# Kernel optimization log

Measured on AMD Instinct MI355X. Metric: run time of the kernel, lower is better.

Reference implementation:

```python
import jax, jax.numpy as jnp
import numpy as np

M = 4096        # reference column size (init kwarg m)
TAU = 1.0       # temperature
SLICE_LEN = 4096


def setup_inputs() -> dict:
    key = jax.random.key(0)
    scores = jax.random.normal(key, (4, 131072), dtype=jnp.float32)
    return {"scores": scores}


def reference(scores):
    B, n = scores.shape
    m = min(M, n)
    # global top-m (sorted descending, matching torch.topk sorted=True)
    ref_val, ref_idx = jax.lax.top_k(scores, m)          # (B, m), (B, m)

    n_chunks = n // SLICE_LEN
    # (n_chunks, B, SLICE_LEN): scan over token chunks so only one
    # (B, SLICE_LEN, m) pairwise block is live at a time, as in the torch loop.
    chunks = jnp.swapaxes(scores.reshape(B, n_chunks, SLICE_LEN), 0, 1)

    def step(_, slice_scores):
        # pairwise = -|s_i - ref_j| / tau  -> softmax over m -> argmax -> gather
        pairwise = -jnp.abs(slice_scores[..., None] - ref_val[:, None, :]) / TAU
        P_hat = jax.nn.softmax(pairwise, axis=-1)        # (B, SLICE_LEN, m)
        col_rank = jnp.argmax(P_hat, axis=-1)            # (B, SLICE_LEN)
        perm_slice = jnp.take_along_axis(ref_idx, col_rank, axis=1)
        return None, perm_slice

    _, perms = jax.lax.scan(step, None, chunks)          # (n_chunks, B, SLICE_LEN)
    perm = jnp.swapaxes(perms, 0, 1).reshape(B, n)       # (B, n) int32 indices
    return perm
```

## Files before the change

### kernel.cpp

```cpp
#include <hip/hip_runtime.h>
#include <stdint.h>

#define BROWS 4
#define NCOLS 131072
#define MREF  4096
#define HIST_BITS 13
#define NBUCK (1 << HIST_BITS)
#define USHIFT (32 - HIST_BITS)
#define CAP 6144
#define HIST_BLK_PER_ROW 8
#define NPART 32
#define PQUOTA 192
#define PARTCAP 1024

__device__ __forceinline__ uint32_t orderable(float f) {
    uint32_t u = __float_as_uint(f);
    return (u & 0x80000000u) ? ~u : (u | 0x80000000u);
}
__device__ __forceinline__ float unorderable(uint32_t u) {
    uint32_t b = (u & 0x80000000u) ? (u & 0x7FFFFFFFu) : ~u;
    return __uint_as_float(b);
}

__global__ void k_zero(uint32_t* hist) {
    int i = blockIdx.x * blockDim.x + threadIdx.x;
    int tot = BROWS * NBUCK;
    for (; i < tot; i += gridDim.x * blockDim.x) hist[i] = 0u;
}

__global__ void k_hist(const float* __restrict__ sc, uint32_t* __restrict__ hist) {
    __shared__ uint32_t h[NBUCK];
    for (int t = threadIdx.x; t < NBUCK; t += blockDim.x) h[t] = 0u;
    __syncthreads();
    int row  = blockIdx.x / HIST_BLK_PER_ROW;
    int part = blockIdx.x % HIST_BLK_PER_ROW;
    const int CHUNK = NCOLS / HIST_BLK_PER_ROW;
    const float* p = sc + row * NCOLS + part * CHUNK;
    for (int c = threadIdx.x; c < CHUNK; c += blockDim.x) {
        uint32_t u = orderable(p[c]);
        atomicAdd(&h[u >> USHIFT], 1u);
    }
    __syncthreads();
    uint32_t* g = hist + (row << HIST_BITS);
    for (int t = threadIdx.x; t < NBUCK; t += blockDim.x) {
        uint32_t v = h[t];
        if (v) atomicAdd(&g[t], v);
    }
}

__global__ void k_thresh(const uint32_t* __restrict__ hist, uint32_t* __restrict__ Hrow,
                         int* __restrict__ Bs, uint32_t* __restrict__ pcur,
                         uint32_t* __restrict__ pse) {
    __shared__ uint32_t inc[256];
    int row = blockIdx.x;
    const uint32_t* h = hist + (row << HIST_BITS);
    int bhi = NBUCK - 1 - (int)threadIdx.x * 32;
    uint32_t run = 0;
    for (int k = 0; k < 32; ++k) run += h[bhi - k];
    inc[threadIdx.x] = run;
    __syncthreads();
    for (int off = 1; off < 256; off <<= 1) {
        uint32_t v = (threadIdx.x >= (uint32_t)off) ? inc[threadIdx.x - off] : 0u;
        __syncthreads();
        inc[threadIdx.x] += v;
        __syncthreads();
    }
    uint32_t excl = inc[threadIdx.x] - run;

    if (threadIdx.x == 0) {
        Bs[row * NPART + 0] = NBUCK;
        pcur[row * NPART + 0] = 0u;
        pse[row * (NPART + 1) + 0] = 0u;
    }

    uint32_t cum = excl;
    for (int k = 0; k < 32; ++k) {
        int b = bhi - k;
        uint32_t prev = cum;
        cum += h[b];
        if (prev < (uint32_t)MREF) {
            uint32_t plo = prev / PQUOTA + 1u;
            uint32_t phi = cum / PQUOTA;
            if (phi > (uint32_t)(NPART - 1)) phi = (uint32_t)(NPART - 1);
            for (uint32_t p = plo; p <= phi; ++p) {
                uint32_t st = prev; if (st > (uint32_t)CAP) st = (uint32_t)CAP;
                Bs[row * NPART + p] = b;
                pcur[row * NPART + p] = st;
                pse[row * (NPART + 1) + p] = st;
            }
            if (cum >= (uint32_t)MREF) {
                uint32_t T = cum; if (T > (uint32_t)CAP) T = (uint32_t)CAP;
                Hrow[row] = (uint32_t)b;
                pse[row * (NPART + 1) + NPART] = T;
                uint32_t pstart = cum / PQUOTA + 1u;
                for (uint32_t p = pstart; p < (uint32_t)NPART; ++p) {
                    Bs[row * NPART + p] = b - 1;
                    pcur[row * NPART + p] = T;
                    pse[row * (NPART + 1) + p] = T;
                }
            }
        }
    }
}

__global__ void k_compact(const float* __restrict__ sc, const uint32_t* __restrict__ Hrow,
                          const int* __restrict__ Bs, uint32_t* __restrict__ pcur,
                          uint64_t* __restrict__ cand) {
    __shared__ int bsL[NPART];
    __shared__ uint32_t cntP[NPART];
    __shared__ uint32_t baseP[NPART];
    int row = blockIdx.x >> 7;
    int base = (blockIdx.x & 127) << 10;
    uint32_t H = Hrow[row];
    if (threadIdx.x < NPART) {
        bsL[threadIdx.x] = Bs[row * NPART + threadIdx.x];
        cntP[threadIdx.x] = 0u;
    }
    __syncthreads();
    const float* p = sc + row * NCOLS + base;

    uint32_t myu[4], mycol[4], myr[4];
    int myp[4];
    uint32_t n = 0;
    for (int k = 0; k < 4; ++k) {
        int c = (int)threadIdx.x + (k << 8);
        uint32_t u = orderable(p[c]);
        uint32_t b = u >> USHIFT;
        if (b >= H) {
            int pp = 0;
            for (int q = 1; q < NPART; ++q) pp += ((int)b <= bsL[q]) ? 1 : 0;
            myu[n] = u; mycol[n] = (uint32_t)(base + c); myp[n] = pp;
            myr[n] = atomicAdd(&cntP[pp], 1u);
            ++n;
        }
    }
    __syncthreads();
    if (threadIdx.x < NPART)
        baseP[threadIdx.x] = atomicAdd(&pcur[row * NPART + threadIdx.x], cntP[threadIdx.x]);
    __syncthreads();
    uint64_t* cr = cand + (size_t)row * CAP;
    for (uint32_t k = 0; k < n; ++k) {
        uint32_t idx = baseP[myp[k]] + myr[k];
        if (idx < (uint32_t)CAP)
            cr[idx] = ((uint64_t)(~myu[k]) << 32) | mycol[k];
    }
}

#define BITONIC_SORT(PP)                                                        \
    for (uint32_t i = threadIdx.x; i < (uint32_t)(PP); i += blockDim.x)         \
        lds[i] = (i < n) ? seg[i] : ~0ULL;                                      \
    __syncthreads();                                                            \
    for (uint32_t k = 2; k <= (uint32_t)(PP); k <<= 1) {                        \
        for (uint32_t j = k >> 1; j > 0; j >>= 1) {                             \
            for (uint32_t i = threadIdx.x; i < (uint32_t)(PP); i += blockDim.x) { \
                uint32_t ixj = i ^ j;                                           \
                if (ixj > i) {                                                  \
                    uint64_t a = lds[i], bb = lds[ixj];                         \
                    bool up = ((i & k) == 0);                                   \
                    if ((a > bb) == up) { lds[i] = bb; lds[ixj] = a; }          \
                }                                                               \
            }                                                                   \
            __syncthreads();                                                    \
        }                                                                       \
    }

__global__ void k_psort(const uint32_t* __restrict__ pse, uint64_t* __restrict__ cand,
                        float* __restrict__ rv, uint32_t* __restrict__ ri) {
    __shared__ uint64_t lds[PARTCAP];
    int row = blockIdx.x >> 5;
    int pp  = blockIdx.x & 31;
    uint32_t start = pse[row * (NPART + 1) + pp];
    uint32_t end   = pse[row * (NPART + 1) + pp + 1];
    if (end > (uint32_t)CAP) end = (uint32_t)CAP;
    uint32_t n = (end > start) ? (end - start) : 0u;
    if (n > (uint32_t)PARTCAP) n = (uint32_t)PARTCAP;
    uint64_t* seg = cand + (size_t)row * CAP + start;
    if (n <= 256u) {
        BITONIC_SORT(256)
    } else if (n <= 512u) {
        BITONIC_SORT(512)
    } else {
        BITONIC_SORT(1024)
    }
    for (uint32_t i = threadIdx.x; i < n; i += blockDim.x) {
        uint32_t gpos = start + i;
        if (gpos < (uint32_t)MREF) {
            uint64_t key = lds[i];
            uint32_t u = ~(uint32_t)(key >> 32);
            rv[row * MREF + gpos] = unorderable(u);
            ri[row * MREF + gpos] = (uint32_t)(key & 0xFFFFFFFFu);
        }
    }
}

__global__ void k_map(const float* __restrict__ sc, const float* __restrict__ rv,
                      const uint32_t* __restrict__ ri, int* __restrict__ out) {
    __shared__ float srv[MREF];
    int row = blockIdx.x >> 9;
    int col = ((blockIdx.x & 511) << 8) + threadIdx.x;
    const float* rvr = rv + row * MREF;
    for (int t = threadIdx.x; t < MREF; t += blockDim.x) srv[t] = rvr[t];
    __syncthreads();

    float s = sc[row * NCOLS + col];
    int lo = 0, hi = MREF;
    while (lo < hi) { int mid = (lo + hi) >> 1; if (srv[mid] <= s) hi = mid; else lo = mid + 1; }
    int p = lo, jmin;
    if (p == 0) jmin = 0;
    else if (p == MREF) jmin = MREF - 1;
    else {
        float dp = fabsf(s - srv[p]);
        float dm = fabsf(s - srv[p - 1]);
        jmin = (dm <= dp) ? (p - 1) : p;
    }
    float pmax = -fabsf(s - srv[jmin]);
    int jans = jmin;
    for (int j = jmin - 1; j >= 0; --j) {
        float pw = -fabsf(s - srv[j]);
        if (expf(pw - pmax) == 1.0f) jans = j; else break;
    }
    out[row * NCOLS + col] = (int)ri[row * MREF + jans];
}

extern "C" void kernel_launch(void* const* d_in, const int* in_sizes, int n_in,
                              void* d_out, int out_size, void* d_ws, size_t ws_size,
                              hipStream_t stream) {
    const float* sc = (const float*)d_in[0];
    int* out = (int*)d_out;
    char* w = (char*)d_ws;

    uint32_t* hist = (uint32_t*)w;
    uint32_t* Hrow = (uint32_t*)(w + 131072);
    int*      Bs   = (int*)     (w + 131200);
    uint32_t* pcur = (uint32_t*)(w + 131712);
    uint32_t* pse  = (uint32_t*)(w + 132224);
    uint64_t* cand = (uint64_t*)(w + 132864);
    float*    rv   = (float*)   (w + 329472);
    uint32_t* ri   = (uint32_t*)(w + 395008);

    k_zero   <<<64, 256, 0, stream>>>(hist);
    k_hist   <<<BROWS * HIST_BLK_PER_ROW, 256, 0, stream>>>(sc, hist);
    k_thresh <<<BROWS, 256, 0, stream>>>(hist, Hrow, Bs, pcur, pse);
    k_compact<<<512, 256, 0, stream>>>(sc, Hrow, Bs, pcur, cand);
    k_psort  <<<BROWS * NPART, 512, 0, stream>>>(pse, cand, rv, ri);
    k_map    <<<BROWS * 512, 256, 0, stream>>>(sc, rv, ri, out);
}
```

Measured before the change: 66.59 us.

## Fuse histogram and threshold kernels via last-block-done counter, widen histogram grid

Merges the histogram and threshold-selection kernels into one launch. Each block bumps a per-row atomic counter, and the last block to finish computes the prefix scan over the global histogram. The zeroing kernel becomes a hipMemsetAsync that also clears the counters. Histogram blocks per row double to 16 with 512 threads per block, which spreads the input read across more CUs. This removes two kernel launches at the cost of more global atomic merges and a serialized tail in the last block.

```diff
diff --git a/kernel.cpp b/kernel.cpp
--- a/kernel.cpp
+++ b/kernel.cpp
@@ -8,7 +8,7 @@
 #define NBUCK (1 << HIST_BITS)
 #define USHIFT (32 - HIST_BITS)
 #define CAP 6144
-#define HIST_BLK_PER_ROW 8
+#define HIST_BLK_PER_ROW 16
 #define NPART 32
 #define PQUOTA 192
 #define PARTCAP 1024
@@ -21,82 +21,84 @@
     uint32_t b = (u & 0x80000000u) ? (u & 0x7FFFFFFFu) : ~u;
     return __uint_as_float(b);
 }
-
-__global__ void k_zero(uint32_t* hist) {
-    int i = blockIdx.x * blockDim.x + threadIdx.x;
-    int tot = BROWS * NBUCK;
-    for (; i < tot; i += gridDim.x * blockDim.x) hist[i] = 0u;
-}
-
-__global__ void k_hist(const float* __restrict__ sc, uint32_t* __restrict__ hist) {
+__device__ __forceinline__ uint32_t gload(const uint32_t* p) {
+    return __hip_atomic_load(p, __ATOMIC_RELAXED, __HIP_MEMORY_SCOPE_AGENT);
+}
+
+__global__ void k_histthresh(const float* __restrict__ sc, uint32_t* __restrict__ hist,
+                             uint32_t* __restrict__ cnt, uint32_t* __restrict__ Hrow,
+                             int* __restrict__ Bs, uint32_t* __restrict__ pcur,
+                             uint32_t* __restrict__ pse) {
     __shared__ uint32_t h[NBUCK];
-    for (int t = threadIdx.x; t < NBUCK; t += blockDim.x) h[t] = 0u;
-    __syncthreads();
-    int row  = blockIdx.x / HIST_BLK_PER_ROW;
-    int part = blockIdx.x % HIST_BLK_PER_ROW;
+    __shared__ uint32_t inc[512];
+    __shared__ uint32_t lastflag;
+    const int tid = (int)threadIdx.x;
+    for (int t = tid; t < NBUCK; t += 512) h[t] = 0u;
+    __syncthreads();
+    int row  = (int)blockIdx.x / HIST_BLK_PER_ROW;
+    int part = (int)blockIdx.x % HIST_BLK_PER_ROW;
     const int CHUNK = NCOLS / HIST_BLK_PER_ROW;
     const float* p = sc + row * NCOLS + part * CHUNK;
-    for (int c = threadIdx.x; c < CHUNK; c += blockDim.x) {
+    for (int c = tid; c < CHUNK; c += 512) {
         uint32_t u = orderable(p[c]);
         atomicAdd(&h[u >> USHIFT], 1u);
     }
     __syncthreads();
     uint32_t* g = hist + (row << HIST_BITS);
-    for (int t = threadIdx.x; t < NBUCK; t += blockDim.x) {
+    for (int t = tid; t < NBUCK; t += 512) {
         uint32_t v = h[t];
         if (v) atomicAdd(&g[t], v);
     }
-}
-
-__global__ void k_thresh(const uint32_t* __restrict__ hist, uint32_t* __restrict__ Hrow,
-                         int* __restrict__ Bs, uint32_t* __restrict__ pcur,
-                         uint32_t* __restrict__ pse) {
-    __shared__ uint32_t inc[256];
-    int row = blockIdx.x;
-    const uint32_t* h = hist + (row << HIST_BITS);
-    int bhi = NBUCK - 1 - (int)threadIdx.x * 32;
+    __syncthreads();
+    if (tid == 0) {
+        __threadfence();
+        lastflag = atomicAdd(&cnt[row * 32], 1u);
+    }
+    __syncthreads();
+    if (lastflag != (uint32_t)(HIST_BLK_PER_ROW - 1)) return;
+    __threadfence();
+
+    int bhi = NBUCK - 1 - tid * 16;
     uint32_t run = 0;
-    for (int k = 0; k < 32; ++k) run += h[bhi - k];
-    inc[threadIdx.x] = run;
-    __syncthreads();
-    for (int off = 1; off < 256; off <<= 1) {
-        uint32_t v = (threadIdx.x >= (uint32_t)off) ? inc[threadIdx.x - off] : 0u;
+    for (int k = 0; k < 16; ++k) run += gload(&g[bhi - k]);
+    inc[tid] = run;
+    __syncthreads();
+    for (int off = 1; off < 512; off <<= 1) {
+        uint32_t v = (tid >= off) ? inc[tid - off] : 0u;
         __syncthreads();
-        inc[threadIdx.x] += v;
+        inc[tid] += v;
         __syncthreads();
     }
-    uint32_t excl = inc[threadIdx.x] - run;
-
-    if (threadIdx.x == 0) {
+    uint32_t excl = inc[tid] - run;
+    if (tid == 0) {
         Bs[row * NPART + 0] = NBUCK;
         pcur[row * NPART + 0] = 0u;
         pse[row * (NPART + 1) + 0] = 0u;
     }
-
     uint32_t cum = excl;
-    for (int k = 0; k < 32; ++k) {
+    for (int k = 0; k < 16; ++k) {
         int b = bhi - k;
         uint32_t prev = cum;
-        cum += h[b];
+        cum += gload(&g[b]);
         if (prev < (uint32_t)MREF) {
             uint32_t plo = prev / PQUOTA + 1u;
             uint32_t phi = cum / PQUOTA;
             if (phi > (uint32_t)(NPART - 1)) phi = (uint32_t)(NPART - 1);
-            for (uint32_t p = plo; p <= phi; ++p) {
+            for (uint32_t pq = plo; pq <= phi; ++pq) {
                 uint32_t st = prev; if (st > (uint32_t)CAP) st = (uint32_t)CAP;
-                Bs[row * NPART + p] = b;
-                pcur[row * NPART + p] = st;
-                pse[row * (NPART + 1) + p] = st;
+                Bs[row * NPART + pq] = b;
+                pcur[row * NPART + pq] = st;
+                pse[row * (NPART + 1) + pq] = st;
             }
             if (cum >= (uint32_t)MREF) {
                 uint32_t T = cum; if (T > (uint32_t)CAP) T = (uint32_t)CAP;
                 Hrow[row] = (uint32_t)b;
                 pse[row * (NPART + 1) + NPART] = T;
                 uint32_t pstart = cum / PQUOTA + 1u;
-                for (uint32_t p = pstart; p < (uint32_t)NPART; ++p) {
-                    Bs[row * NPART + p] = b - 1;
-                    pcur[row * NPART + p] = T;
-                    pse[row * (NPART + 1) + p] = T;
+                for (uint32_t pq = pstart; pq < (uint32_t)NPART; ++pq) {
+                    Bs[row * NPART + pq] = b - 1;
+                    pcur[row * NPART + pq] = T;
+                    pse[row * (NPART + 1) + pq] = T;
                 }
             }
         }
@@ -230,18 +232,18 @@
     char* w = (char*)d_ws;
 
     uint32_t* hist = (uint32_t*)w;
-    uint32_t* Hrow = (uint32_t*)(w + 131072);
-    int*      Bs   = (int*)     (w + 131200);
-    uint32_t* pcur = (uint32_t*)(w + 131712);
-    uint32_t* pse  = (uint32_t*)(w + 132224);
-    uint64_t* cand = (uint64_t*)(w + 132864);
-    float*    rv   = (float*)   (w + 329472);
-    uint32_t* ri   = (uint32_t*)(w + 395008);
-
-    k_zero   <<<64, 256, 0, stream>>>(hist);
-    k_hist   <<<BROWS * HIST_BLK_PER_ROW, 256, 0, stream>>>(sc, hist);
-    k_thresh <<<BROWS, 256, 0, stream>>>(hist, Hrow, Bs, pcur, pse);
-    k_compact<<<512, 256, 0, stream>>>(sc, Hrow, Bs, pcur, cand);
-    k_psort  <<<BROWS * NPART, 512, 0, stream>>>(pse, cand, rv, ri);
-    k_map    <<<BROWS * 512, 256, 0, stream>>>(sc, rv, ri, out);
-}
+    uint32_t* cnt  = (uint32_t*)(w + 131072);
+    uint32_t* Hrow = (uint32_t*)(w + 131584);
+    int*      Bs   = (int*)     (w + 131712);
+    uint32_t* pcur = (uint32_t*)(w + 132224);
+    uint32_t* pse  = (uint32_t*)(w + 132736);
+    uint64_t* cand = (uint64_t*)(w + 133376);
+    float*    rv   = (float*)   (w + 329984);
+    uint32_t* ri   = (uint32_t*)(w + 395520);
+
+    hipMemsetAsync(w, 0, 131072 + 512, stream);
+    k_histthresh<<<BROWS * HIST_BLK_PER_ROW, 512, 0, stream>>>(sc, hist, cnt, Hrow, Bs, pcur, pse);
+    k_compact   <<<512, 256, 0, stream>>>(sc, Hrow, Bs, pcur, cand);
+    k_psort     <<<BROWS * NPART, 512, 0, stream>>>(pse, cand, rv, ri);
+    k_map       <<<BROWS * 512, 256, 0, stream>>>(sc, rv, ri, out);
+}
```

After: 62.49 us. 6.2% less time.
